# Kernel optimization log

Hardware: AMD Instinct MI355X
Metric: run time of the kernel (lower is better)

Reference implementation:

```python
import jax, jax.numpy as jnp
import numpy as np
import math
from jax import lax

L = 16
T = 2 ** 14          # hash table size (power of 2 -> uint32 arithmetic is exact mod T)
F_DIM = 2
N_MIN, N_MAX = 16, 512
_B = math.exp((math.log(N_MAX) - math.log(N_MIN)) / (L - 1))
NS = [int(N_MIN * _B ** i) for i in range(L)]
PRIME = np.uint32(2654435761)


def setup_inputs() -> dict:
    key = jax.random.key(0)
    k1, k2 = jax.random.split(key)
    x = jax.random.uniform(k1, (8, 2, 512, 512), dtype=jnp.float32)
    hash_table = jax.random.uniform(k2, (L, T, F_DIM), dtype=jnp.float32) * 2e-4 - 1e-4
    return {"x": x, "hash_table": hash_table}


def reference(x, hash_table):
    b, c, h, w = x.shape
    feats = []
    for i, n in enumerate(NS):
        kh, kw = h // n, w // n
        # max_pool2d(x*n, (kh,kw), stride=1) -> [b, 2, h-kh+1, w-kw+1]
        g = lax.reduce_window(x * n, -jnp.inf, lax.max,
                              (1, 1, kh, kw), (1, 1, 1, 1), 'VALID')
        g = g.astype(jnp.uint32)  # trunc toward zero, values nonneg and small
        # prime-XOR hash; T is a power of two so uint32 wraparound matches int64 math mod T
        idx = (g[:, 0] ^ (g[:, 1] * PRIME)) % np.uint32(T)  # [b, gh, gw]
        f = hash_table[i][idx]                 # gather -> [b, gh, gw, F_DIM]
        f = jnp.transpose(f, (0, 3, 1, 2))     # [b, F_DIM, gh, gw]
        # bilinear upsample (half-pixel centers == align_corners=False)
        f = jax.image.resize(f, (b, F_DIM, h, w), method='bilinear')
        feats.append(f)
    return jnp.concatenate(feats, axis=1)       # [b, L*F_DIM, h, w]
```

## Files before the change

kernel.cpp:

```cpp
#include <hip/hip_runtime.h>
#include <stdint.h>

#define NLVL 16
#define TSIZE 16384
#define HW 512

typedef float vfloat4 __attribute__((ext_vector_type(4)));

__constant__ int c_n[NLVL] = {16,20,25,32,40,50,64,80,101,128,161,203,256,322,406,512};

__device__ __forceinline__ uint32_t pkmax(uint32_t a, uint32_t b) {
    uint32_t r;
    asm("v_pk_max_u16 %0, %1, %2" : "=v"(r) : "v"(a), "v"(b));
    return r;
}

template<int K>
__device__ __forceinline__ void do_tile(
        const int lvl, const int b, const int tx0, const int ty0,
        const float* __restrict__ x, const float* __restrict__ table,
        float* __restrict__ out, uint32_t* lds) {
    constexpr int gh = 513 - K;
    constexpr float s = (float)gh * (1.0f / 512.0f);
    const float nf = (float)c_n[lvl];
    const int tid = threadIdx.x;

    const float* xb0 = x + (size_t)b * 2 * HW * HW;
    const float* xb1 = xb0 + HW * HW;
    const float2* tb = (const float2*)table + (size_t)lvl * TSIZE;
    float* ob = out + ((size_t)b * 32 + lvl * 2) * HW * HW;

    if constexpr (K == 1) {
        const int oy = tid >> 3, xo = tx0 + (tid & 7) * 4;
        const int y = ty0 + oy;
        const float4 v0 = *(const float4*)&xb0[y * HW + xo];
        const float4 v1 = *(const float4*)&xb1[y * HW + xo];
        vfloat4 o0, o1;
        {
            const uint32_t i0 = (((uint32_t)(v0.x * nf)) ^ (((uint32_t)(v1.x * nf)) * 2654435761u)) & (TSIZE - 1);
            const uint32_t i1 = (((uint32_t)(v0.y * nf)) ^ (((uint32_t)(v1.y * nf)) * 2654435761u)) & (TSIZE - 1);
            const uint32_t i2 = (((uint32_t)(v0.z * nf)) ^ (((uint32_t)(v1.z * nf)) * 2654435761u)) & (TSIZE - 1);
            const uint32_t i3 = (((uint32_t)(v0.w * nf)) ^ (((uint32_t)(v1.w * nf)) * 2654435761u)) & (TSIZE - 1);
            const float2 f0 = tb[i0], f1 = tb[i1], f2 = tb[i2], f3 = tb[i3];
            o0 = (vfloat4){f0.x, f1.x, f2.x, f3.x};
            o1 = (vfloat4){f0.y, f1.y, f2.y, f3.y};
        }
        const size_t o = (size_t)y * HW + xo;
        __builtin_nontemporal_store(o0, (vfloat4*)&ob[o]);
        __builtin_nontemporal_store(o1, (vfloat4*)&ob[o + (size_t)HW * HW]);
        return;
    }

    uint32_t* V   = lds;
    float2*  feat = (float2*)(lds + 33 * 68);

    const int gy_base = (int)floorf(((float)ty0 + 0.5f) * s - 0.5f);
    const int gx_base = (int)floorf(((float)tx0 + 0.5f) * s - 0.5f);
    const int rmin = max(gy_base, 0);
    const int cmin = max(gx_base, 0);

    {
        const int wv = __builtin_amdgcn_readfirstlane(tid >> 6);
        const int c  = tid & 63;
        const int r0 = 8 * wv;
        const int xx = min(cmin + c, HW - 1);
        const int ybase = rmin + r0;
        uint32_t e[K + 8];
#pragma unroll
        for (int t = 0; t < K + 8; ++t) {
            const int yy = min(ybase + t, HW - 1);
            const float v0 = (xb0 + yy * HW)[xx];
            const float v1 = (xb1 + yy * HW)[xx];
            e[t] = (uint32_t)(v0 * nf) | ((uint32_t)(v1 * nf) << 16);
        }
        uint32_t o[9];
        if constexpr (K >= 10) {
            uint32_t sfx[9];
            sfx[8] = e[8];
#pragma unroll
            for (int t = 7; t >= 0; --t) sfx[t] = pkmax(e[t], sfx[t + 1]);
            uint32_t run = e[9];
#pragma unroll
            for (int m = 9; m <= K + 7; ++m) {
                if (m > 9) run = pkmax(run, e[m]);
                if (m >= K - 1) o[m - K + 1] = pkmax(sfx[m - K + 1], run);
            }
        } else {
#pragma unroll
            for (int i = 0; i < 9; ++i) {
                uint32_t m = e[i];
#pragma unroll
                for (int t = 1; t < K; ++t) m = pkmax(m, e[i + t]);
                o[i] = m;
            }
        }
        const int vb = r0 * 68 + c;
#pragma unroll
        for (int t = 0; t < 9; ++t) V[vb + t * 68] = o[t];
    }
    __syncthreads();

    if (tid < 99) {
        const int i = tid / 3, g = tid % 3;
        constexpr int NE  = 12 + K - 1;
        constexpr int NCH = (NE + 3) >> 2;
        uint32_t f[NCH * 4];
        const uint4* rp = (const uint4*)(V + i * 68 + 12 * g);
#pragma unroll
        for (int cc = 0; cc < NCH; ++cc) {
            const uint4 q = rp[cc];
            f[4*cc] = q.x; f[4*cc+1] = q.y; f[4*cc+2] = q.z; f[4*cc+3] = q.w;
        }
        uint32_t wm[12];
        if constexpr (K >= 13) {
            uint32_t sfx[12];
            sfx[11] = f[11];
#pragma unroll
            for (int d = 10; d >= 0; --d) sfx[d] = pkmax(f[d], sfx[d + 1]);
            uint32_t run = f[12];
#pragma unroll
            for (int m = 12; m <= K + 10; ++m) {
                if (m > 12) run = pkmax(run, f[m]);
                if (m >= K - 1) wm[m - K + 1] = pkmax(sfx[m - K + 1], run);
            }
        } else {
#pragma unroll
            for (int d = 0; d < 12; ++d) {
                uint32_t m = f[d];
#pragma unroll
                for (int t = 1; t < K; ++t) m = pkmax(m, f[d + t]);
                wm[d] = m;
            }
        }
#pragma unroll
        for (int d = 0; d < 12; ++d) {
            const int j = 12 * g + d;
            if (j < 33) {
                const uint32_t m = wm[d];
                const uint32_t idx = ((m & 0xFFFFu) ^ ((m >> 16) * 2654435761u)) & (TSIZE - 1);
                feat[i * 34 + j] = tb[idx];
            }
        }
    }
    __syncthreads();

    const int bty = tid >> 5, btx = tid & 31;
    const int xo = tx0 + btx;
    const float sxf = ((float)xo + 0.5f) * s - 0.5f;
    const float fxf = floorf(sxf);
    const float wx = sxf - fxf;
    const int x0i = (int)fxf;
    const int jx0 = min(max(x0i, 0), gh - 1) - cmin;
    const int jx1 = min(max(x0i + 1, 0), gh - 1) - cmin;
    for (int oy = bty; oy < 32; oy += 8) {
        const int y = ty0 + oy;
        const float syf = ((float)y + 0.5f) * s - 0.5f;
        const float fyf = floorf(syf);
        const float wy = syf - fyf;
        const int y0i = (int)fyf;
        const int iy0 = min(max(y0i, 0), gh - 1) - rmin;
        const int iy1 = min(max(y0i + 1, 0), gh - 1) - rmin;
        const float2 f00 = feat[iy0 * 34 + jx0], f01 = feat[iy0 * 34 + jx1];
        const float2 f10 = feat[iy1 * 34 + jx0], f11 = feat[iy1 * 34 + jx1];
        const float w11 = wy * wx;
        const float w10 = wy - w11;
        const float w01 = wx - w11;
        const float w00 = 1.0f - wy - wx + w11;
        const float c0 = f00.x * w00 + f01.x * w01 + f10.x * w10 + f11.x * w11;
        const float c1 = f00.y * w00 + f01.y * w01 + f10.y * w10 + f11.y * w11;
        const size_t o = (size_t)y * HW + xo;
        __builtin_nontemporal_store(c0, &ob[o]);
        __builtin_nontemporal_store(c1, &ob[o + (size_t)HW * HW]);
    }
}

__global__ __launch_bounds__(256) void fused_kernel(
        const float* __restrict__ x, const float* __restrict__ table,
        float* __restrict__ out) {
    __shared__ __align__(16) uint32_t lds[33 * 68 + 33 * 34 * 2];

    const int bid  = blockIdx.x;
    const int b    = bid & 7;
    const int half = (bid >> 3) & 1;
    const int tile = (bid >> 4) & 255;
    const int pair = bid >> 12;
    const int lvl  = pair + 8 * half;
    const int tx0  = (tile & 15) * 32;
    const int ty0  = (tile >> 4) * 32;

    switch (lvl) {
        case  0: do_tile<32>( 0, b, tx0, ty0, x, table, out, lds); break;
        case  1: do_tile<25>( 1, b, tx0, ty0, x, table, out, lds); break;
        case  2: do_tile<20>( 2, b, tx0, ty0, x, table, out, lds); break;
        case  3: do_tile<16>( 3, b, tx0, ty0, x, table, out, lds); break;
        case  4: do_tile<12>( 4, b, tx0, ty0, x, table, out, lds); break;
        case  5: do_tile<10>( 5, b, tx0, ty0, x, table, out, lds); break;
        case  6: do_tile< 8>( 6, b, tx0, ty0, x, table, out, lds); break;
        case  7: do_tile< 6>( 7, b, tx0, ty0, x, table, out, lds); break;
        case  8: do_tile< 5>( 8, b, tx0, ty0, x, table, out, lds); break;
        case  9: do_tile< 4>( 9, b, tx0, ty0, x, table, out, lds); break;
        case 10: do_tile< 3>(10, b, tx0, ty0, x, table, out, lds); break;
        case 11: do_tile< 2>(11, b, tx0, ty0, x, table, out, lds); break;
        case 12: do_tile< 2>(12, b, tx0, ty0, x, table, out, lds); break;
        case 13: do_tile< 1>(13, b, tx0, ty0, x, table, out, lds); break;
        case 14: do_tile< 1>(14, b, tx0, ty0, x, table, out, lds); break;
        default: do_tile< 1>(15, b, tx0, ty0, x, table, out, lds); break;
    }
}

extern "C" void kernel_launch(void* const* d_in, const int* in_sizes, int n_in,
                              void* d_out, int out_size, void* d_ws, size_t ws_size,
                              hipStream_t stream) {
    const float* x     = (const float*)d_in[0];
    const float* table = (const float*)d_in[1];
    float* out         = (float*)d_out;
    (void)d_ws; (void)ws_size;

    fused_kernel<<<dim3(NLVL * 256 * 8), dim3(256), 0, stream>>>(x, table, out);
}
```

Before: 110.2 us.

## Process level pairs per block and merge the three identity levels

Each block now handles two hash-grid levels in sequence instead of one, halving the grid size. The three finest levels (pool size 1) are merged into one routine that loads the input tile once and produces all three outputs. This is meant to cut block launch overhead and redundant input reads. In exchange, the per-block work becomes uneven across groups, with the coarse-level pairs much heavier than the others, which may create tail imbalance.

New measurement: 111.7 us. About the same (+1.4%).

```diff
diff --git a/kernel.cpp b/kernel.cpp
--- a/kernel.cpp
+++ b/kernel.cpp
@@ -29,27 +29,6 @@
     const float* xb1 = xb0 + HW * HW;
     const float2* tb = (const float2*)table + (size_t)lvl * TSIZE;
     float* ob = out + ((size_t)b * 32 + lvl * 2) * HW * HW;
-
-    if constexpr (K == 1) {
-        const int oy = tid >> 3, xo = tx0 + (tid & 7) * 4;
-        const int y = ty0 + oy;
-        const float4 v0 = *(const float4*)&xb0[y * HW + xo];
-        const float4 v1 = *(const float4*)&xb1[y * HW + xo];
-        vfloat4 o0, o1;
-        {
-            const uint32_t i0 = (((uint32_t)(v0.x * nf)) ^ (((uint32_t)(v1.x * nf)) * 2654435761u)) & (TSIZE - 1);
-            const uint32_t i1 = (((uint32_t)(v0.y * nf)) ^ (((uint32_t)(v1.y * nf)) * 2654435761u)) & (TSIZE - 1);
-            const uint32_t i2 = (((uint32_t)(v0.z * nf)) ^ (((uint32_t)(v1.z * nf)) * 2654435761u)) & (TSIZE - 1);
-            const uint32_t i3 = (((uint32_t)(v0.w * nf)) ^ (((uint32_t)(v1.w * nf)) * 2654435761u)) & (TSIZE - 1);
-            const float2 f0 = tb[i0], f1 = tb[i1], f2 = tb[i2], f3 = tb[i3];
-            o0 = (vfloat4){f0.x, f1.x, f2.x, f3.x};
-            o1 = (vfloat4){f0.y, f1.y, f2.y, f3.y};
-        }
-        const size_t o = (size_t)y * HW + xo;
-        __builtin_nontemporal_store(o0, (vfloat4*)&ob[o]);
-        __builtin_nontemporal_store(o1, (vfloat4*)&ob[o + (size_t)HW * HW]);
-        return;
-    }
 
     uint32_t* V   = lds;
     float2*  feat = (float2*)(lds + 33 * 68);
@@ -174,6 +153,36 @@
     }
 }
 
+__device__ __forceinline__ void identity3(
+        const int b, const int tx0, const int ty0,
+        const float* __restrict__ x, const float* __restrict__ table,
+        float* __restrict__ out) {
+    const int tid = threadIdx.x;
+    const int oy = tid >> 3, xo = tx0 + (tid & 7) * 4;
+    const int y = ty0 + oy;
+    const float* xb0 = x + (size_t)b * 2 * HW * HW;
+    const float* xb1 = xb0 + HW * HW;
+    const float4 v0 = *(const float4*)&xb0[y * HW + xo];
+    const float4 v1 = *(const float4*)&xb1[y * HW + xo];
+    const size_t o = (size_t)y * HW + xo;
+#pragma unroll
+    for (int li = 0; li < 3; ++li) {
+        const int lvl = 13 + li;
+        const float nf = (float)c_n[13 + li];
+        const float2* tb = (const float2*)table + (size_t)lvl * TSIZE;
+        float* ob = out + ((size_t)b * 32 + lvl * 2) * HW * HW;
+        const uint32_t i0 = (((uint32_t)(v0.x * nf)) ^ (((uint32_t)(v1.x * nf)) * 2654435761u)) & (TSIZE - 1);
+        const uint32_t i1 = (((uint32_t)(v0.y * nf)) ^ (((uint32_t)(v1.y * nf)) * 2654435761u)) & (TSIZE - 1);
+        const uint32_t i2 = (((uint32_t)(v0.z * nf)) ^ (((uint32_t)(v1.z * nf)) * 2654435761u)) & (TSIZE - 1);
+        const uint32_t i3 = (((uint32_t)(v0.w * nf)) ^ (((uint32_t)(v1.w * nf)) * 2654435761u)) & (TSIZE - 1);
+        const float2 f0 = tb[i0], f1 = tb[i1], f2 = tb[i2], f3 = tb[i3];
+        const vfloat4 o0 = (vfloat4){f0.x, f1.x, f2.x, f3.x};
+        const vfloat4 o1 = (vfloat4){f0.y, f1.y, f2.y, f3.y};
+        __builtin_nontemporal_store(o0, (vfloat4*)&ob[o]);
+        __builtin_nontemporal_store(o1, (vfloat4*)&ob[o + (size_t)HW * HW]);
+    }
+}
+
 __global__ __launch_bounds__(256) void fused_kernel(
         const float* __restrict__ x, const float* __restrict__ table,
         float* __restrict__ out) {
@@ -181,30 +190,26 @@
 
     const int bid  = blockIdx.x;
     const int b    = bid & 7;
-    const int half = (bid >> 3) & 1;
-    const int tile = (bid >> 4) & 255;
-    const int pair = bid >> 12;
-    const int lvl  = pair + 8 * half;
+    const int tile = (bid >> 3) & 255;
+    const int grp  = bid >> 11;
     const int tx0  = (tile & 15) * 32;
     const int ty0  = (tile >> 4) * 32;
 
-    switch (lvl) {
-        case  0: do_tile<32>( 0, b, tx0, ty0, x, table, out, lds); break;
-        case  1: do_tile<25>( 1, b, tx0, ty0, x, table, out, lds); break;
-        case  2: do_tile<20>( 2, b, tx0, ty0, x, table, out, lds); break;
-        case  3: do_tile<16>( 3, b, tx0, ty0, x, table, out, lds); break;
-        case  4: do_tile<12>( 4, b, tx0, ty0, x, table, out, lds); break;
-        case  5: do_tile<10>( 5, b, tx0, ty0, x, table, out, lds); break;
-        case  6: do_tile< 8>( 6, b, tx0, ty0, x, table, out, lds); break;
-        case  7: do_tile< 6>( 7, b, tx0, ty0, x, table, out, lds); break;
-        case  8: do_tile< 5>( 8, b, tx0, ty0, x, table, out, lds); break;
-        case  9: do_tile< 4>( 9, b, tx0, ty0, x, table, out, lds); break;
-        case 10: do_tile< 3>(10, b, tx0, ty0, x, table, out, lds); break;
-        case 11: do_tile< 2>(11, b, tx0, ty0, x, table, out, lds); break;
-        case 12: do_tile< 2>(12, b, tx0, ty0, x, table, out, lds); break;
-        case 13: do_tile< 1>(13, b, tx0, ty0, x, table, out, lds); break;
-        case 14: do_tile< 1>(14, b, tx0, ty0, x, table, out, lds); break;
-        default: do_tile< 1>(15, b, tx0, ty0, x, table, out, lds); break;
+    switch (grp) {
+        case 0: do_tile<32>( 0, b, tx0, ty0, x, table, out, lds);
+                do_tile<25>( 1, b, tx0, ty0, x, table, out, lds); break;
+        case 1: do_tile<20>( 2, b, tx0, ty0, x, table, out, lds);
+                do_tile<16>( 3, b, tx0, ty0, x, table, out, lds); break;
+        case 2: do_tile<12>( 4, b, tx0, ty0, x, table, out, lds);
+                do_tile<10>( 5, b, tx0, ty0, x, table, out, lds); break;
+        case 3: do_tile< 8>( 6, b, tx0, ty0, x, table, out, lds);
+                do_tile< 6>( 7, b, tx0, ty0, x, table, out, lds); break;
+        case 4: do_tile< 5>( 8, b, tx0, ty0, x, table, out, lds);
+                do_tile< 4>( 9, b, tx0, ty0, x, table, out, lds); break;
+        case 5: do_tile< 3>(10, b, tx0, ty0, x, table, out, lds);
+                do_tile< 2>(11, b, tx0, ty0, x, table, out, lds); break;
+        case 6: do_tile< 2>(12, b, tx0, ty0, x, table, out, lds); break;
+        default: identity3(b, tx0, ty0, x, table, out); break;
     }
 }
 
@@ -216,5 +221,5 @@
     float* out         = (float*)d_out;
     (void)d_ws; (void)ws_size;
 
-    fused_kernel<<<dim3(NLVL * 256 * 8), dim3(256), 0, stream>>>(x, table, out);
-}
+    fused_kernel<<<dim3(8 * 256 * 8), dim3(256), 0, stream>>>(x, table, out);
+}
```
